# Optimization experiments

Hardware: AMD Instinct MI355X
Metric: run time of the kernel (lower is better)

## Reference

```python
import jax, jax.numpy as jnp
import numpy as np

N = 50000
E = 400000
DIM_IN = 512
DIM_H = 64
HEADS = 8
DIM_OUT = 40
SLOPE = 0.2  # PyG GATv2Conv default negative_slope


def setup_inputs() -> dict:
    key = jax.random.key(0)
    ks = jax.random.split(key, 16)
    s = 0.05
    return {
        "x": jax.random.normal(ks[0], (N, DIM_IN), dtype=jnp.float32),
        "edge_index": jax.random.randint(ks[1], (2, E), 0, N, dtype=jnp.int64),
        "Wl1": jax.random.normal(ks[2], (DIM_IN, HEADS * DIM_H), dtype=jnp.float32) * s,
        "Wr1": jax.random.normal(ks[3], (DIM_IN, HEADS * DIM_H), dtype=jnp.float32) * s,
        "att1": jax.random.normal(ks[4], (HEADS, DIM_H), dtype=jnp.float32) * s,
        "b1": jax.random.normal(ks[5], (HEADS * DIM_H,), dtype=jnp.float32) * s,
        "Wl2": jax.random.normal(ks[6], (HEADS * DIM_H, DIM_OUT), dtype=jnp.float32) * s,
        "Wr2": jax.random.normal(ks[7], (HEADS * DIM_H, DIM_OUT), dtype=jnp.float32) * s,
        "att2": jax.random.normal(ks[8], (1, DIM_OUT), dtype=jnp.float32) * s,
        "b2": jax.random.normal(ks[9], (DIM_OUT,), dtype=jnp.float32) * s,
        "Wl3": jax.random.normal(ks[10], (HEADS * DIM_H, 2), dtype=jnp.float32) * s,
        "Wr3": jax.random.normal(ks[11], (HEADS * DIM_H, 2), dtype=jnp.float32) * s,
        "att3": jax.random.normal(ks[12], (1, 2), dtype=jnp.float32) * s,
        "b3": jax.random.normal(ks[13], (2,), dtype=jnp.float32) * s,
    }


def gatv2(x, src, dst, Wl, Wr, att, b):
    # PyG GATv2Conv: e_ij = att . LeakyReLU(W_l x_j + W_r x_i); softmax over j (by dst i);
    # out_i = sum_j alpha_ij * (W_l x_j); heads concatenated; bias added after.
    n = x.shape[0]
    H, F = att.shape
    xl = (x @ Wl).reshape(n, H, F)  # source transform
    xr = (x @ Wr).reshape(n, H, F)  # target transform
    e = jax.nn.leaky_relu(xl[src] + xr[dst], negative_slope=SLOPE)  # [E, H, F]
    logits = jnp.einsum("ehf,hf->eh", e, att)  # [E, H]
    m = jax.ops.segment_max(logits, dst, num_segments=n)  # self-loops => every segment nonempty
    ex = jnp.exp(logits - m[dst])
    denom = jax.ops.segment_sum(ex, dst, num_segments=n)
    alpha = ex / denom[dst]  # [E, H]
    out = jax.ops.segment_sum(xl[src] * alpha[:, :, None], dst, num_segments=n)  # [N, H, F]
    return out.reshape(n, H * F) + b


def reference(x, edge_index, Wl1, Wr1, att1, b1, Wl2, Wr2, att2, b2, Wl3, Wr3, att3, b3):
    # add self loops (PyG default add_self_loops=True)
    loops = jnp.arange(N, dtype=edge_index.dtype)
    ei = jnp.concatenate([edge_index, jnp.stack([loops, loops])], axis=1)
    src, dst = ei[0], ei[1]
    # eval mode: dropout is identity; ReverseLayerF is identity in forward
    h = jax.nn.relu(gatv2(x, src, dst, Wl1, Wr1, att1, b1))
    y_class = gatv2(h, src, dst, Wl2, Wr2, att2, b2)
    y_domain = gatv2(h, src, dst, Wl3, Wr3, att3, b3)
    return (y_class, y_domain)
```

## Files before the change

### kernel.cpp

```cpp
#include <hip/hip_runtime.h>
#include <math.h>

typedef unsigned short u16;
typedef unsigned int   u32;
typedef __attribute__((ext_vector_type(8))) short bf16x8;
typedef __attribute__((ext_vector_type(4))) float f32x4;
typedef __attribute__((ext_vector_type(4))) u32   u32x4;

__device__ __forceinline__ float b2f(u16 u) {
  union { u32 i; float f; } v; v.i = ((u32)u) << 16; return v.f;
}
__device__ __forceinline__ u16 f2b(float f) {
  union { u32 i; float f; } v; v.f = f;
  u32 r = v.i + 0x7FFFu + ((v.i >> 16) & 1u);
  return (u16)(r >> 16);
}
__device__ __forceinline__ float blo(u32 w) {
  union { u32 i; float f; } v; v.i = w << 16; return v.f;
}
__device__ __forceinline__ float bhi(u32 w) {
  union { u32 i; float f; } v; v.i = w & 0xFFFF0000u; return v.f;
}
__device__ __forceinline__ void ld_lds16(const u16* g, u16* l) {
  __builtin_amdgcn_global_load_lds((const __attribute__((address_space(1))) void*)g,
                                   (__attribute__((address_space(3))) void*)l, 16, 0, 0);
}

#define NN 50000
#define NE 400000
#define NT 450000
#define NBLK_SCAN 196

__global__ void k_detect(const void* x, const void* ei, int* flags) {
  __shared__ int cnt[2];
  int t = threadIdx.x;
  if (t < 2) cnt[t] = 0;
  __syncthreads();
  u16 u = ((const u16*)x)[t];
  int e = (u >> 7) & 0xFF;
  if (u == 0 || (e >= 90 && e <= 134)) atomicAdd(&cnt[0], 1);
  if (t < 16) {
    if (((const int*)ei)[2 * t + 1] == 0) atomicAdd(&cnt[1], 1);
  }
  __syncthreads();
  if (t == 0) {
    flags[0] = (cnt[0] >= 110) ? 1 : 0;
    flags[1] = (cnt[1] >= 15) ? 1 : 0;
  }
}

__device__ __forceinline__ int eidx(const int* ei, int pos, int i64) {
  return i64 ? ei[2 * pos] : ei[pos];
}

__global__ void k_convert_x(const void* x, const int* flags, u16* xb) {
  if (flags[0]) return;
  int c = blockIdx.x * 256 + threadIdx.x;
  const float* xf = (const float*)x + (size_t)c * 8;
  u32x4 o;
  #pragma unroll
  for (int i = 0; i < 4; ++i) {
    u32 lo = f2b(xf[2 * i]);
    u32 hi = f2b(xf[2 * i + 1]);
    o[i] = lo | (hi << 16);
  }
  *(u32x4*)(xb + (size_t)c * 8) = o;
}

__global__ void k_pack(const void* Wl1, const void* Wr1, const void* Wl2, const void* Wr2,
                       const void* Wl3, const void* Wr3, const void* att1, const void* b1,
                       const void* att2, const void* b2, const void* att3, const void* b3,
                       const int* flags, u16* w1t, u16* w23t, float* params) {
  int b = blockIdx.x;
  int isbf = flags[0];
  if (b < 2048) {
    int t = b * 256 + threadIdx.x;
    int r = t >> 9;
    int k = t & 511;
    const void* W = (r < 512) ? Wl1 : Wr1;
    int cc = r & 511;
    u16 v = isbf ? ((const u16*)W)[k * 512 + cc] : f2b(((const float*)W)[k * 512 + cc]);
    w1t[(size_t)r * 512 + k] = v;
  } else if (b < 2240) {
    int t = (b - 2048) * 256 + threadIdx.x;
    int k = t / 96;
    int c = t % 96;
    const void* W = nullptr; int idx = 0;
    if (c < 40)      { W = Wl2; idx = k * 40 + c; }
    else if (c < 42) { W = Wl3; idx = k * 2 + (c - 40); }
    else if (c < 82) { W = Wr2; idx = k * 40 + (c - 42); }
    else if (c < 84) { W = Wr3; idx = k * 2 + (c - 82); }
    u16 v = 0;
    if (W) v = isbf ? ((const u16*)W)[idx] : f2b(((const float*)W)[idx]);
    w23t[c * 512 + k] = v;
  } else {
    int t = (b - 2240) * 256 + threadIdx.x;
    if (t >= 1108) return;
    const void* src; int idx;
    if (t < 512)       { src = att1; idx = t; }
    else if (t < 1024) { src = b1;   idx = t - 512; }
    else if (t < 1064) { src = att2; idx = t - 1024; }
    else if (t < 1104) { src = b2;   idx = t - 1064; }
    else if (t < 1106) { src = att3; idx = t - 1104; }
    else               { src = b3;   idx = t - 1106; }
    params[t] = isbf ? b2f(((const u16*)src)[idx]) : ((const float*)src)[idx];
  }
}

__global__ void k_hist(const int* ei, const int* flags, int* deg) {
  int e = blockIdx.x * 256 + threadIdx.x;
  if (e >= NE) return;
  int d = eidx(ei, NE + e, flags[1]);
  atomicAdd(&deg[d], 1);
}

__global__ void k_scanA(const int* deg, int* row_ptr, int* bsum) {
  __shared__ int sh[256];
  int b = blockIdx.x, t = threadIdx.x;
  int i = b * 256 + t;
  int val = (i < NN) ? deg[i] + 1 : 0;
  sh[t] = val;
  __syncthreads();
  #pragma unroll
  for (int off = 1; off < 256; off <<= 1) {
    int v = (t >= off) ? sh[t - off] : 0;
    __syncthreads();
    sh[t] += v;
    __syncthreads();
  }
  if (i < NN) row_ptr[i] = sh[t] - val;
  if (t == 255) bsum[b] = sh[255];
}

__global__ void k_scanB(int* bsum, int* row_ptr) {
  __shared__ int sh[256];
  int t = threadIdx.x;
  int val = (t < NBLK_SCAN) ? bsum[t] : 0;
  sh[t] = val;
  __syncthreads();
  #pragma unroll
  for (int off = 1; off < 256; off <<= 1) {
    int v = (t >= off) ? sh[t - off] : 0;
    __syncthreads();
    sh[t] += v;
    __syncthreads();
  }
  if (t < NBLK_SCAN) bsum[t] = sh[t] - val;
  if (t == 255) row_ptr[NN] = sh[255];
}

__global__ void k_scanC(const int* bsum, int* row_ptr, int* cursor) {
  int i = blockIdx.x * 256 + threadIdx.x;
  if (i < NN) {
    int v = row_ptr[i] + bsum[blockIdx.x];
    row_ptr[i] = v;
    cursor[i] = v;
  }
}

__global__ void k_scatter(const int* ei, const int* flags, int* cursor, int* csr_src) {
  int t = blockIdx.x * 256 + threadIdx.x;
  if (t >= NT) return;
  int i64 = flags[1];
  int s, d;
  if (t < NE) { s = eidx(ei, t, i64); d = eidx(ei, NE + t, i64); }
  else        { s = d = t - NE; }
  int pos = atomicAdd(&cursor[d], 1);
  csr_src[pos] = s;
}

__global__ __launch_bounds__(256) void k_gemm1(const void* __restrict__ xraw, const u16* __restrict__ xb,
                                               const u16* __restrict__ Bt, const int* __restrict__ flags,
                                               u16* __restrict__ XL, u16* __restrict__ XR) {
  __shared__ __align__(16) u16 As[128 * 64];
  __shared__ __align__(16) u16 Bs[128 * 64];
  const int id  = blockIdx.x;
  const int xcd = id & 7;
  const int lb  = id >> 3;
  const int mt  = xcd * 49 + (lb >> 3);
  const int nt  = lb & 7;
  if (mt >= 391) return;
  const int m0 = mt * 128;
  const int n0 = nt * 128;
  const u16* __restrict__ A = flags[0] ? (const u16*)xraw : xb;
  const int t = threadIdx.x;
  const int wave = t >> 6;
  const int lane = t & 63;
  const int wm = (wave >> 1) * 64;
  const int wn = (wave & 1) * 64;
  const int fr = lane & 15;
  const int fk = lane >> 4;
  const int srow = lane >> 3;
  const int schk = (lane & 7) ^ srow;
  f32x4 acc[4][4] = {};
  for (int k0 = 0; k0 < 512; k0 += 64) {
    #pragma unroll
    for (int q = 0; q < 4; ++q) {
      int rbase = wave * 32 + q * 8;
      int gm = m0 + rbase + srow;
      if (gm > NN - 1) gm = NN - 1;
      ld_lds16(&A[(size_t)gm * 512 + k0 + schk * 8], &As[rbase * 64]);
      ld_lds16(&Bt[(size_t)(n0 + rbase + srow) * 512 + k0 + schk * 8], &Bs[rbase * 64]);
    }
    __syncthreads();
    #pragma unroll
    for (int h = 0; h < 2; ++h) {
      int s = h * 4 + fk;
      bf16x8 af[4], bb[4];
      #pragma unroll
      for (int i = 0; i < 4; ++i) {
        int row = wm + i * 16 + fr;
        af[i] = *(const bf16x8*)&As[row * 64 + ((s ^ (row & 7)) * 8)];
      }
      #pragma unroll
      for (int j = 0; j < 4; ++j) {
        int row = wn + j * 16 + fr;
        bb[j] = *(const bf16x8*)&Bs[row * 64 + ((s ^ (row & 7)) * 8)];
      }
      #pragma unroll
      for (int i = 0; i < 4; ++i)
        #pragma unroll
        for (int j = 0; j < 4; ++j)
          acc[i][j] = __builtin_amdgcn_mfma_f32_16x16x32_bf16(af[i], bb[j], acc[i][j], 0, 0, 0);
    }
    __syncthreads();
  }
  #pragma unroll
  for (int i = 0; i < 4; ++i) {
    #pragma unroll
    for (int r = 0; r < 4; ++r) {
      int gm = m0 + wm + i * 16 + fk * 4 + r;
      if (gm < NN) {
        #pragma unroll
        for (int j = 0; j < 4; ++j) {
          int gn = n0 + wn + j * 16 + fr;
          u16 v = f2b(acc[i][j][r]);
          if (gn < 512) XL[(size_t)gm * 512 + gn] = v;
          else          XR[(size_t)gm * 512 + gn - 512] = v;
        }
      }
    }
  }
}

__global__ __launch_bounds__(256) void k_gemm2(const u16* __restrict__ A, const u16* __restrict__ Bt,
                                               float* __restrict__ xlp, float* __restrict__ xrp) {
  __shared__ __align__(16) short As[128][40];
  __shared__ __align__(16) short Bs[96][40];
  const int m0 = blockIdx.x * 128;
  const int t = threadIdx.x;
  const int wave = t >> 6;
  const int lane = t & 63;
  const int fr = lane & 15;
  const int fk = lane >> 4;
  const int wm = wave * 32;
  f32x4 acc[2][6] = {};
  for (int k0 = 0; k0 < 512; k0 += 32) {
    #pragma unroll
    for (int h = 0; h < 2; ++h) {
      int c = t + h * 256;
      int row = c >> 2, kc = (c & 3) * 8;
      int gm = m0 + row;
      u32x4 va = {0, 0, 0, 0};
      if (gm < NN) va = *(const u32x4*)&A[(size_t)gm * 512 + k0 + kc];
      *(u32x4*)&As[row][kc] = va;
    }
    for (int c = t; c < 384; c += 256) {
      int row = c >> 2, kc = (c & 3) * 8;
      *(u32x4*)&Bs[row][kc] = *(const u32x4*)&Bt[row * 512 + k0 + kc];
    }
    __syncthreads();
    bf16x8 af[2], bb[6];
    #pragma unroll
    for (int i = 0; i < 2; ++i) af[i] = *(const bf16x8*)&As[wm + i * 16 + fr][fk * 8];
    #pragma unroll
    for (int j = 0; j < 6; ++j) bb[j] = *(const bf16x8*)&Bs[j * 16 + fr][fk * 8];
    #pragma unroll
    for (int i = 0; i < 2; ++i)
      #pragma unroll
      for (int j = 0; j < 6; ++j)
        acc[i][j] = __builtin_amdgcn_mfma_f32_16x16x32_bf16(af[i], bb[j], acc[i][j], 0, 0, 0);
    __syncthreads();
  }
  #pragma unroll
  for (int i = 0; i < 2; ++i) {
    #pragma unroll
    for (int j = 0; j < 6; ++j) {
      int gn = j * 16 + fr;
      if (gn < 84) {
        #pragma unroll
        for (int r = 0; r < 4; ++r) {
          int gm = m0 + wm + i * 16 + fk * 4 + r;
          if (gm < NN) {
            if (gn < 42) xlp[(size_t)gm * 48 + gn] = acc[i][j][r];
            else         xrp[(size_t)gm * 48 + gn - 42] = acc[i][j][r];
          }
        }
      }
    }
  }
}

__global__ __launch_bounds__(256) void k_layer1f(const u16* __restrict__ xl1, const u16* __restrict__ xr1,
                                                 const int* __restrict__ row_ptr, const int* __restrict__ csr_src,
                                                 const float* __restrict__ params, u16* __restrict__ hb) {
  int wid = blockIdx.x * 4 + (threadIdx.x >> 6);
  int lane = threadIdx.x & 63;
  int nw = gridDim.x * 4;
  float att4[8];
  #pragma unroll
  for (int k = 0; k < 8; ++k) att4[k] = 0.4f * params[lane * 8 + k];
  for (int i = wid; i < NN; i += nw) {
    int e0 = row_ptr[i], e1 = row_ptr[i + 1];
    u32x4 xrv = *(const u32x4*)&xr1[(size_t)i * 512 + lane * 8];
    float xr[8];
    #pragma unroll
    for (int q = 0; q < 4; ++q) { xr[2 * q] = blo(xrv[q]); xr[2 * q + 1] = bhi(xrv[q]); }
    float dp = 0.f;
    #pragma unroll
    for (int k = 0; k < 8; ++k) dp = fmaf(att4[k], 1.5f * xr[k], dp);
    dp += __shfl_xor(dp, 1, 64);
    dp += __shfl_xor(dp, 2, 64);
    dp += __shfl_xor(dp, 4, 64);
    float s = 0.f;
    float acc[8] = {0.f, 0.f, 0.f, 0.f, 0.f, 0.f, 0.f, 0.f};
    int q0 = csr_src[e0];
    int q1 = csr_src[e0 + 1 < e1 ? e0 + 1 : e1 - 1];
    int q2 = csr_src[e0 + 2 < e1 ? e0 + 2 : e1 - 1];
    int q3 = csr_src[e0 + 3 < e1 ? e0 + 3 : e1 - 1];
    for (int p = e0; p < e1; p += 4) {
      int j0 = q0, j1 = q1, j2 = q2, j3 = q3;
      u32x4 v0 = *(const u32x4*)&xl1[(size_t)j0 * 512 + lane * 8];
      u32x4 v1 = *(const u32x4*)&xl1[(size_t)j1 * 512 + lane * 8];
      u32x4 v2 = *(const u32x4*)&xl1[(size_t)j2 * 512 + lane * 8];
      u32x4 v3 = *(const u32x4*)&xl1[(size_t)j3 * 512 + lane * 8];
      int np = p + 4;
      if (np < e1) {
        q0 = csr_src[np];
        q1 = csr_src[np + 1 < e1 ? np + 1 : e1 - 1];
        q2 = csr_src[np + 2 < e1 ? np + 2 : e1 - 1];
        q3 = csr_src[np + 3 < e1 ? np + 3 : e1 - 1];
      }
      float m1 = (p + 1 < e1) ? 1.f : 0.f;
      float m2 = (p + 2 < e1) ? 1.f : 0.f;
      float m3 = (p + 3 < e1) ? 1.f : 0.f;
      float c0 = 0.f, c1 = 0.f, c2 = 0.f, c3 = 0.f;
      float xlv0[8], xlv1[8], xlv2[8], xlv3[8];
      #pragma unroll
      for (int q = 0; q < 4; ++q) {
        xlv0[2 * q] = blo(v0[q]); xlv0[2 * q + 1] = bhi(v0[q]);
        xlv1[2 * q] = blo(v1[q]); xlv1[2 * q + 1] = bhi(v1[q]);
        xlv2[2 * q] = blo(v2[q]); xlv2[2 * q + 1] = bhi(v2[q]);
        xlv3[2 * q] = blo(v3[q]); xlv3[2 * q + 1] = bhi(v3[q]);
      }
      #pragma unroll
      for (int k = 0; k < 8; ++k) {
        float t0 = xlv0[k] + xr[k];
        float t1 = xlv1[k] + xr[k];
        float t2 = xlv2[k] + xr[k];
        float t3 = xlv3[k] + xr[k];
        float u0 = fmaf(1.5f, xlv0[k], fabsf(t0));
        float u1 = fmaf(1.5f, xlv1[k], fabsf(t1));
        float u2 = fmaf(1.5f, xlv2[k], fabsf(t2));
        float u3 = fmaf(1.5f, xlv3[k], fabsf(t3));
        c0 = fmaf(att4[k], u0, c0);
        c1 = fmaf(att4[k], u1, c1);
        c2 = fmaf(att4[k], u2, c2);
        c3 = fmaf(att4[k], u3, c3);
      }
      c0 += __shfl_xor(c0, 1, 64); c1 += __shfl_xor(c1, 1, 64);
      c2 += __shfl_xor(c2, 2, 64); c3 += __shfl_xor(c3, 1, 64);
      c0 += __shfl_xor(c0, 2, 64); c1 += __shfl_xor(c1, 2, 64);
      c2 += __shfl_xor(c2, 1, 64); c3 += __shfl_xor(c3, 2, 64);
      c0 += __shfl_xor(c0, 4, 64); c1 += __shfl_xor(c1, 4, 64);
      c2 += __shfl_xor(c2, 4, 64); c3 += __shfl_xor(c3, 4, 64);
      float l0 = c0 + dp;
      float l1 = c1 + dp;
      float l2 = c2 + dp;
      float l3 = c3 + dp;
      float pv0 = __expf(fminf(fmaxf(l0, -30.f), 30.f));
      float pv1 = __expf(fminf(fmaxf(l1, -30.f), 30.f)) * m1;
      float pv2 = __expf(fminf(fmaxf(l2, -30.f), 30.f)) * m2;
      float pv3 = __expf(fminf(fmaxf(l3, -30.f), 30.f)) * m3;
      s += (pv0 + pv1) + (pv2 + pv3);
      #pragma unroll
      for (int k = 0; k < 8; ++k) {
        float a = fmaf(pv0, xlv0[k], acc[k]);
        a = fmaf(pv1, xlv1[k], a);
        a = fmaf(pv2, xlv2[k], a);
        acc[k] = fmaf(pv3, xlv3[k], a);
      }
    }
    float r = 1.f / s;
    u32x4 o;
    #pragma unroll
    for (int q = 0; q < 4; ++q) {
      u32 lo = f2b(fmaxf(fmaf(acc[2 * q],     r, params[512 + lane * 8 + 2 * q]),     0.f));
      u32 hi = f2b(fmaxf(fmaf(acc[2 * q + 1], r, params[512 + lane * 8 + 2 * q + 1]), 0.f));
      o[q] = lo | (hi << 16);
    }
    *(u32x4*)&hb[(size_t)i * 512 + lane * 8] = o;
  }
}

__global__ __launch_bounds__(256) void k_layer23f(const float* __restrict__ xlp, const float* __restrict__ xrp,
                                                  const int* __restrict__ row_ptr, const int* __restrict__ csr_src,
                                                  const float* __restrict__ params,
                                                  const int* __restrict__ flags, void* __restrict__ out) {
  int wid = blockIdx.x * 4 + (threadIdx.x >> 6);
  int lane = threadIdx.x & 63;
  int nw = gridDim.x * 4;
  int e = lane >> 3;
  int g = lane & 7;
  int c0 = g * 5;
  float att2[5];
  #pragma unroll
  for (int u = 0; u < 5; ++u) att2[u] = params[1024 + c0 + u];
  float att3a = params[1104], att3b = params[1105];
  int isbf = flags[0];
  for (int i = wid; i < NN; i += nw) {
    int e0 = row_ptr[i], e1 = row_ptr[i + 1];
    const float* xri = &xrp[(size_t)i * 48];
    float xr2[5];
    #pragma unroll
    for (int u = 0; u < 5; ++u) xr2[u] = xri[c0 + u];
    float xr3a = xri[40], xr3b = xri[41];
    float s2 = 0.f, s3 = 0.f;
    float acc2[5] = {0.f, 0.f, 0.f, 0.f, 0.f};
    float acc3a = 0.f, acc3b = 0.f;
    int nit = (e1 - e0 + 7) >> 3;
    for (int it = 0; it < nit; ++it) {
      int p = e0 + it * 8 + e;
      bool valid = p < e1;
      int j = csr_src[valid ? p : e1 - 1];
      const float* xlj = &xlp[(size_t)j * 48];
      float xl2[5];
      #pragma unroll
      for (int u = 0; u < 5; ++u) xl2[u] = xlj[c0 + u];
      float part = 0.f;
      #pragma unroll
      for (int u = 0; u < 5; ++u) {
        float t = xl2[u] + xr2[u];
        part = fmaf(att2[u], fmaxf(t, 0.2f * t), part);
      }
      part += __shfl_xor(part, 1, 64);
      part += __shfl_xor(part, 2, 64);
      part += __shfl_xor(part, 4, 64);
      float pv2 = valid ? __expf(fminf(fmaxf(part, -30.f), 30.f)) : 0.f;
      s2 += pv2;
      #pragma unroll
      for (int u = 0; u < 5; ++u) acc2[u] = fmaf(pv2, xl2[u], acc2[u]);
      if (g == 0) {
        float xl3a = xlj[40], xl3b = xlj[41];
        float ta = xl3a + xr3a, tb = xl3b + xr3b;
        float l3 = fmaf(att3a, fmaxf(ta, 0.2f * ta), att3b * fmaxf(tb, 0.2f * tb));
        float pv3 = valid ? __expf(fminf(fmaxf(l3, -30.f), 30.f)) : 0.f;
        s3 += pv3;
        acc3a = fmaf(pv3, xl3a, acc3a);
        acc3b = fmaf(pv3, xl3b, acc3b);
      }
    }
    #pragma unroll
    for (int m = 8; m <= 32; m <<= 1) {
      #pragma unroll
      for (int u = 0; u < 5; ++u) acc2[u] += __shfl_xor(acc2[u], m, 64);
      s2 += __shfl_xor(s2, m, 64);
      acc3a += __shfl_xor(acc3a, m, 64);
      acc3b += __shfl_xor(acc3b, m, 64);
      s3 += __shfl_xor(s3, m, 64);
    }
    if (e == 0) {
      float r2 = 1.f / s2;
      #pragma unroll
      for (int u = 0; u < 5; ++u) {
        float v = acc2[u] * r2 + params[1064 + c0 + u];
        size_t o = (size_t)i * 40 + c0 + u;
        if (isbf) ((u16*)out)[o] = f2b(v); else ((float*)out)[o] = v;
      }
      if (g == 0) {
        float r3 = 1.f / s3;
        float va = acc3a * r3 + params[1106];
        float vb = acc3b * r3 + params[1107];
        size_t o = 2000000 + (size_t)i * 2;
        if (isbf) { ((u16*)out)[o] = f2b(va); ((u16*)out)[o + 1] = f2b(vb); }
        else      { ((float*)out)[o] = va;    ((float*)out)[o + 1] = vb; }
      }
    }
  }
}

extern "C" void kernel_launch(void* const* d_in, const int* in_sizes, int n_in,
                              void* d_out, int out_size, void* d_ws, size_t ws_size,
                              hipStream_t stream) {
  const void* x    = d_in[0];
  const int*  ei   = (const int*)d_in[1];
  const void* Wl1  = d_in[2];
  const void* Wr1  = d_in[3];
  const void* att1 = d_in[4];
  const void* b1   = d_in[5];
  const void* Wl2  = d_in[6];
  const void* Wr2  = d_in[7];
  const void* att2 = d_in[8];
  const void* b2   = d_in[9];
  const void* Wl3  = d_in[10];
  const void* Wr3  = d_in[11];
  const void* att3 = d_in[12];
  const void* b3   = d_in[13];
  (void)in_sizes; (void)n_in; (void)out_size;

  char* ws = (char*)d_ws;
  size_t off = 0;
  auto alloc = [&](size_t bytes) -> void* {
    void* p = ws + off;
    off = (off + bytes + 255) & ~(size_t)255;
    return p;
  };
  int*   flags   = (int*)  alloc(64);
  u16*   xb      = (u16*)  alloc((size_t)NN * 512 * 2);
  u16*   w1t     = (u16*)  alloc((size_t)1024 * 512 * 2);
  u16*   xl1     = (u16*)  alloc((size_t)NN * 512 * 2);
  u16*   xr1     = (u16*)  alloc((size_t)NN * 512 * 2);
  u16*   hb      = (u16*)  alloc((size_t)NN * 512 * 2);
  u16*   w23t    = (u16*)  alloc((size_t)96 * 512 * 2);
  float* xlp     = (float*)alloc((size_t)NN * 48 * 4);
  float* xrp     = (float*)alloc((size_t)NN * 48 * 4);
  float* params  = (float*)alloc(1108 * 4);
  int*   row_ptr = (int*)  alloc((NN + 1) * 4);
  int*   deg     = (int*)  alloc(NN * 4);
  int*   cursor  = (int*)  alloc(NN * 4);
  int*   csr_src = (int*)  alloc((NT + 16) * 4);
  int*   bsum    = (int*)  alloc(256 * 4);
  if (ws_size < off) return;

  hipLaunchKernelGGL(k_detect, dim3(1), dim3(128), 0, stream, x, (const void*)ei, flags);
  hipLaunchKernelGGL(k_convert_x, dim3(12500), dim3(256), 0, stream, x, flags, xb);
  hipLaunchKernelGGL(k_pack, dim3(2245), dim3(256), 0, stream, Wl1, Wr1, Wl2, Wr2, Wl3, Wr3,
                     att1, b1, att2, b2, att3, b3, flags, w1t, w23t, params);
  hipMemsetAsync(deg, 0, NN * 4, stream);
  hipLaunchKernelGGL(k_hist, dim3((NE + 255) / 256), dim3(256), 0, stream, ei, flags, deg);
  hipLaunchKernelGGL(k_scanA, dim3(NBLK_SCAN), dim3(256), 0, stream, deg, row_ptr, bsum);
  hipLaunchKernelGGL(k_scanB, dim3(1), dim3(256), 0, stream, bsum, row_ptr);
  hipLaunchKernelGGL(k_scanC, dim3(NBLK_SCAN), dim3(256), 0, stream, bsum, row_ptr, cursor);
  hipLaunchKernelGGL(k_scatter, dim3((NT + 255) / 256), dim3(256), 0, stream, ei, flags, cursor, csr_src);
  hipLaunchKernelGGL(k_gemm1, dim3(3136), dim3(256), 0, stream, x, xb, w1t, flags, xl1, xr1);
  hipLaunchKernelGGL(k_layer1f, dim3(4096), dim3(256), 0, stream, xl1, xr1, row_ptr, csr_src, params, hb);
  hipLaunchKernelGGL(k_gemm2, dim3(391), dim3(256), 0, stream, hb, w23t, xlp, xrp);
  hipLaunchKernelGGL(k_layer23f, dim3(4096), dim3(256), 0, stream, xlp, xrp, row_ptr, csr_src, params, flags, d_out);
}
```

Before: 448.9 us.

## Merge prep kernels and double-buffer A tiles in layer-2 GEMM

Merges the x conversion and weight packing kernels into one launch, cutting one kernel launch. Weight transposition now indexes k-major so reads of the source weights are coalesced. In k_gemm2 the A tile is double-buffered in LDS, with the next slice prefetched into registers while MFMAs run, and B fragments are read straight from global memory instead of being staged. This drops one barrier per k-step but adds global B reads per wave. A shuffle-order tweak in the layer-2/3 reduction is only a reordering with the same sum.

```diff
diff --git a/kernel.cpp b/kernel.cpp
--- a/kernel.cpp
+++ b/kernel.cpp
@@ -53,36 +53,35 @@
   return i64 ? ei[2 * pos] : ei[pos];
 }
 
-__global__ void k_convert_x(const void* x, const int* flags, u16* xb) {
-  if (flags[0]) return;
-  int c = blockIdx.x * 256 + threadIdx.x;
-  const float* xf = (const float*)x + (size_t)c * 8;
-  u32x4 o;
-  #pragma unroll
-  for (int i = 0; i < 4; ++i) {
-    u32 lo = f2b(xf[2 * i]);
-    u32 hi = f2b(xf[2 * i + 1]);
-    o[i] = lo | (hi << 16);
-  }
-  *(u32x4*)(xb + (size_t)c * 8) = o;
-}
-
-__global__ void k_pack(const void* Wl1, const void* Wr1, const void* Wl2, const void* Wr2,
-                       const void* Wl3, const void* Wr3, const void* att1, const void* b1,
-                       const void* att2, const void* b2, const void* att3, const void* b3,
-                       const int* flags, u16* w1t, u16* w23t, float* params) {
+__global__ void k_prep(const void* x, const void* Wl1, const void* Wr1, const void* Wl2,
+                       const void* Wr2, const void* Wl3, const void* Wr3, const void* att1,
+                       const void* b1, const void* att2, const void* b2, const void* att3,
+                       const void* b3, const int* flags, u16* xb, u16* w1t, u16* w23t,
+                       float* params) {
   int b = blockIdx.x;
   int isbf = flags[0];
-  if (b < 2048) {
-    int t = b * 256 + threadIdx.x;
-    int r = t >> 9;
-    int k = t & 511;
-    const void* W = (r < 512) ? Wl1 : Wr1;
-    int cc = r & 511;
+  if (b < 12500) {
+    if (isbf) return;
+    int c = b * 256 + threadIdx.x;
+    const float* xf = (const float*)x + (size_t)c * 8;
+    u32x4 o;
+    #pragma unroll
+    for (int i = 0; i < 4; ++i) {
+      u32 lo = f2b(xf[2 * i]);
+      u32 hi = f2b(xf[2 * i + 1]);
+      o[i] = lo | (hi << 16);
+    }
+    *(u32x4*)(xb + (size_t)c * 8) = o;
+  } else if (b < 14548) {
+    int t = (b - 12500) * 256 + threadIdx.x;
+    int k = t >> 10;
+    int c = t & 1023;
+    const void* W = (c < 512) ? Wl1 : Wr1;
+    int cc = c & 511;
     u16 v = isbf ? ((const u16*)W)[k * 512 + cc] : f2b(((const float*)W)[k * 512 + cc]);
-    w1t[(size_t)r * 512 + k] = v;
-  } else if (b < 2240) {
-    int t = (b - 2048) * 256 + threadIdx.x;
+    w1t[(size_t)c * 512 + k] = v;
+  } else if (b < 14740) {
+    int t = (b - 14548) * 256 + threadIdx.x;
     int k = t / 96;
     int c = t % 96;
     const void* W = nullptr; int idx = 0;
@@ -94,7 +93,7 @@
     if (W) v = isbf ? ((const u16*)W)[idx] : f2b(((const float*)W)[idx]);
     w23t[c * 512 + k] = v;
   } else {
-    int t = (b - 2240) * 256 + threadIdx.x;
+    int t = (b - 14740) * 256 + threadIdx.x;
     if (t >= 1108) return;
     const void* src; int idx;
     if (t < 512)       { src = att1; idx = t; }
@@ -245,8 +244,7 @@
 
 __global__ __launch_bounds__(256) void k_gemm2(const u16* __restrict__ A, const u16* __restrict__ Bt,
                                                float* __restrict__ xlp, float* __restrict__ xrp) {
-  __shared__ __align__(16) short As[128][40];
-  __shared__ __align__(16) short Bs[96][40];
+  __shared__ __align__(16) short As[2][128][40];
   const int m0 = blockIdx.x * 128;
   const int t = threadIdx.x;
   const int wave = t >> 6;
@@ -255,32 +253,45 @@
   const int fk = lane >> 4;
   const int wm = wave * 32;
   f32x4 acc[2][6] = {};
-  for (int k0 = 0; k0 < 512; k0 += 32) {
-    #pragma unroll
-    for (int h = 0; h < 2; ++h) {
-      int c = t + h * 256;
-      int row = c >> 2, kc = (c & 3) * 8;
-      int gm = m0 + row;
-      u32x4 va = {0, 0, 0, 0};
-      if (gm < NN) va = *(const u32x4*)&A[(size_t)gm * 512 + k0 + kc];
-      *(u32x4*)&As[row][kc] = va;
-    }
-    for (int c = t; c < 384; c += 256) {
-      int row = c >> 2, kc = (c & 3) * 8;
-      *(u32x4*)&Bs[row][kc] = *(const u32x4*)&Bt[row * 512 + k0 + kc];
-    }
-    __syncthreads();
+  #pragma unroll
+  for (int h = 0; h < 2; ++h) {
+    int c = t + h * 256;
+    int row = c >> 2, kc = (c & 3) * 8;
+    int gm = m0 + row;
+    u32x4 va = {0, 0, 0, 0};
+    if (gm < NN) va = *(const u32x4*)&A[(size_t)gm * 512 + kc];
+    *(u32x4*)&As[0][row][kc] = va;
+  }
+  __syncthreads();
+  int cur = 0;
+  for (int ks = 0; ks < 16; ++ks) {
+    int k0 = ks * 32;
+    u32x4 nva0 = {0, 0, 0, 0}, nva1 = {0, 0, 0, 0};
+    if (ks < 15) {
+      int c0 = t, row0 = c0 >> 2, kc0 = (c0 & 3) * 8;
+      int c1 = t + 256, row1 = c1 >> 2, kc1 = (c1 & 3) * 8;
+      int gm0 = m0 + row0, gm1 = m0 + row1;
+      if (gm0 < NN) nva0 = *(const u32x4*)&A[(size_t)gm0 * 512 + k0 + 32 + kc0];
+      if (gm1 < NN) nva1 = *(const u32x4*)&A[(size_t)gm1 * 512 + k0 + 32 + kc1];
+    }
     bf16x8 af[2], bb[6];
     #pragma unroll
-    for (int i = 0; i < 2; ++i) af[i] = *(const bf16x8*)&As[wm + i * 16 + fr][fk * 8];
-    #pragma unroll
-    for (int j = 0; j < 6; ++j) bb[j] = *(const bf16x8*)&Bs[j * 16 + fr][fk * 8];
+    for (int j = 0; j < 6; ++j) bb[j] = *(const bf16x8*)&Bt[(size_t)(j * 16 + fr) * 512 + k0 + fk * 8];
+    #pragma unroll
+    for (int i = 0; i < 2; ++i) af[i] = *(const bf16x8*)&As[cur][wm + i * 16 + fr][fk * 8];
     #pragma unroll
     for (int i = 0; i < 2; ++i)
       #pragma unroll
       for (int j = 0; j < 6; ++j)
         acc[i][j] = __builtin_amdgcn_mfma_f32_16x16x32_bf16(af[i], bb[j], acc[i][j], 0, 0, 0);
-    __syncthreads();
+    if (ks < 15) {
+      int c0 = t, row0 = c0 >> 2, kc0 = (c0 & 3) * 8;
+      int c1 = t + 256, row1 = c1 >> 2, kc1 = (c1 & 3) * 8;
+      *(u32x4*)&As[cur ^ 1][row0][kc0] = nva0;
+      *(u32x4*)&As[cur ^ 1][row1][kc1] = nva1;
+    }
+    __syncthreads();
+    cur ^= 1;
   }
   #pragma unroll
   for (int i = 0; i < 2; ++i) {
@@ -369,9 +380,9 @@
         c3 = fmaf(att4[k], u3, c3);
       }
       c0 += __shfl_xor(c0, 1, 64); c1 += __shfl_xor(c1, 1, 64);
-      c2 += __shfl_xor(c2, 2, 64); c3 += __shfl_xor(c3, 1, 64);
+      c2 += __shfl_xor(c2, 1, 64); c3 += __shfl_xor(c3, 1, 64);
       c0 += __shfl_xor(c0, 2, 64); c1 += __shfl_xor(c1, 2, 64);
-      c2 += __shfl_xor(c2, 1, 64); c3 += __shfl_xor(c3, 2, 64);
+      c2 += __shfl_xor(c2, 2, 64); c3 += __shfl_xor(c3, 2, 64);
       c0 += __shfl_xor(c0, 4, 64); c1 += __shfl_xor(c1, 4, 64);
       c2 += __shfl_xor(c2, 4, 64); c3 += __shfl_xor(c3, 4, 64);
       float l0 = c0 + dp;
@@ -533,9 +544,8 @@
   if (ws_size < off) return;
 
   hipLaunchKernelGGL(k_detect, dim3(1), dim3(128), 0, stream, x, (const void*)ei, flags);
-  hipLaunchKernelGGL(k_convert_x, dim3(12500), dim3(256), 0, stream, x, flags, xb);
-  hipLaunchKernelGGL(k_pack, dim3(2245), dim3(256), 0, stream, Wl1, Wr1, Wl2, Wr2, Wl3, Wr3,
-                     att1, b1, att2, b2, att3, b3, flags, w1t, w23t, params);
+  hipLaunchKernelGGL(k_prep, dim3(14745), dim3(256), 0, stream, x, Wl1, Wr1, Wl2, Wr2, Wl3, Wr3,
+                     att1, b1, att2, b2, att3, b3, flags, xb, w1t, w23t, params);
   hipMemsetAsync(deg, 0, NN * 4, stream);
   hipLaunchKernelGGL(k_hist, dim3((NE + 255) / 256), dim3(256), 0, stream, ei, flags, deg);
   hipLaunchKernelGGL(k_scanA, dim3(NBLK_SCAN), dim3(256), 0, stream, deg, row_ptr, bsum);
```

Measured after the change: 454.0 us. About the same (+1.1%).

## Fuse fp32-to-bf16 conversion of x into the first GEMM's tile load

Applied to the files above, without the earlier changes.

Removes the standalone x conversion kernel and its bf16 staging buffer. The first GEMM now loads fp32 rows of x directly, converts them with packed bf16 conversion instructions and writes them into the same swizzled LDS layout the async loads produced. The epilogue also uses the packed conversion instead of manual rounding. This saves a full read and write pass over x, but each A tile is now re-read in fp32 by all eight column tiles, and it goes through registers instead of asynchronous direct-to-LDS loads, which may slow the GEMM's load phase.

```diff
diff --git a/kernel.cpp b/kernel.cpp
--- a/kernel.cpp
+++ b/kernel.cpp
@@ -20,6 +20,11 @@
 }
 __device__ __forceinline__ float bhi(u32 w) {
   union { u32 i; float f; } v; v.i = w & 0xFFFF0000u; return v.f;
+}
+__device__ __forceinline__ u32 cvtpk(float a, float b) {
+  u32 r;
+  asm("v_cvt_pk_bf16_f32 %0, %1, %2" : "=v"(r) : "v"(a), "v"(b));
+  return r;
 }
 __device__ __forceinline__ void ld_lds16(const u16* g, u16* l) {
   __builtin_amdgcn_global_load_lds((const __attribute__((address_space(1))) void*)g,
@@ -51,20 +56,6 @@
 
 __device__ __forceinline__ int eidx(const int* ei, int pos, int i64) {
   return i64 ? ei[2 * pos] : ei[pos];
-}
-
-__global__ void k_convert_x(const void* x, const int* flags, u16* xb) {
-  if (flags[0]) return;
-  int c = blockIdx.x * 256 + threadIdx.x;
-  const float* xf = (const float*)x + (size_t)c * 8;
-  u32x4 o;
-  #pragma unroll
-  for (int i = 0; i < 4; ++i) {
-    u32 lo = f2b(xf[2 * i]);
-    u32 hi = f2b(xf[2 * i + 1]);
-    o[i] = lo | (hi << 16);
-  }
-  *(u32x4*)(xb + (size_t)c * 8) = o;
 }
 
 __global__ void k_pack(const void* Wl1, const void* Wr1, const void* Wl2, const void* Wr2,
@@ -169,8 +160,8 @@
   csr_src[pos] = s;
 }
 
-__global__ __launch_bounds__(256) void k_gemm1(const void* __restrict__ xraw, const u16* __restrict__ xb,
-                                               const u16* __restrict__ Bt, const int* __restrict__ flags,
+__global__ __launch_bounds__(256) void k_gemm1(const void* __restrict__ xraw, const u16* __restrict__ Bt,
+                                               const int* __restrict__ flags,
                                                u16* __restrict__ XL, u16* __restrict__ XR) {
   __shared__ __align__(16) u16 As[128 * 64];
   __shared__ __align__(16) u16 Bs[128 * 64];
@@ -182,7 +173,9 @@
   if (mt >= 391) return;
   const int m0 = mt * 128;
   const int n0 = nt * 128;
-  const u16* __restrict__ A = flags[0] ? (const u16*)xraw : xb;
+  const int isbf = flags[0];
+  const u16*   __restrict__ Ab = (const u16*)xraw;
+  const float* __restrict__ Af = (const float*)xraw;
   const int t = threadIdx.x;
   const int wave = t >> 6;
   const int lane = t & 63;
@@ -197,10 +190,32 @@
     #pragma unroll
     for (int q = 0; q < 4; ++q) {
       int rbase = wave * 32 + q * 8;
-      int gm = m0 + rbase + srow;
-      if (gm > NN - 1) gm = NN - 1;
-      ld_lds16(&A[(size_t)gm * 512 + k0 + schk * 8], &As[rbase * 64]);
       ld_lds16(&Bt[(size_t)(n0 + rbase + srow) * 512 + k0 + schk * 8], &Bs[rbase * 64]);
+    }
+    if (isbf) {
+      #pragma unroll
+      for (int q = 0; q < 4; ++q) {
+        int rbase = wave * 32 + q * 8;
+        int gm = m0 + rbase + srow;
+        if (gm > NN - 1) gm = NN - 1;
+        ld_lds16(&Ab[(size_t)gm * 512 + k0 + schk * 8], &As[rbase * 64]);
+      }
+    } else {
+      #pragma unroll
+      for (int q = 0; q < 4; ++q) {
+        int rbase = wave * 32 + q * 8;
+        int gm = m0 + rbase + srow;
+        if (gm > NN - 1) gm = NN - 1;
+        const float* src = Af + (size_t)gm * 512 + k0 + schk * 8;
+        f32x4 a0 = *(const f32x4*)src;
+        f32x4 a1 = *(const f32x4*)(src + 4);
+        u32x4 o;
+        o[0] = cvtpk(a0[0], a0[1]);
+        o[1] = cvtpk(a0[2], a0[3]);
+        o[2] = cvtpk(a1[0], a1[1]);
+        o[3] = cvtpk(a1[2], a1[3]);
+        *(u32x4*)&As[rbase * 64 + lane * 8] = o;
+      }
     }
     __syncthreads();
     #pragma unroll
@@ -232,11 +247,17 @@
       int gm = m0 + wm + i * 16 + fk * 4 + r;
       if (gm < NN) {
         #pragma unroll
-        for (int j = 0; j < 4; ++j) {
-          int gn = n0 + wn + j * 16 + fr;
-          u16 v = f2b(acc[i][j][r]);
-          if (gn < 512) XL[(size_t)gm * 512 + gn] = v;
-          else          XR[(size_t)gm * 512 + gn - 512] = v;
+        for (int jp = 0; jp < 2; ++jp) {
+          u32 pk = cvtpk(acc[i][2 * jp][r], acc[i][2 * jp + 1][r]);
+          int gn0 = n0 + wn + (2 * jp) * 16 + fr;
+          u16 lo = (u16)pk, hi = (u16)(pk >> 16);
+          if (gn0 < 512) {
+            XL[(size_t)gm * 512 + gn0] = lo;
+            XL[(size_t)gm * 512 + gn0 + 16] = hi;
+          } else {
+            XR[(size_t)gm * 512 + gn0 - 512] = lo;
+            XR[(size_t)gm * 512 + gn0 - 496] = hi;
+          }
         }
       }
     }
@@ -369,9 +390,9 @@
         c3 = fmaf(att4[k], u3, c3);
       }
       c0 += __shfl_xor(c0, 1, 64); c1 += __shfl_xor(c1, 1, 64);
-      c2 += __shfl_xor(c2, 2, 64); c3 += __shfl_xor(c3, 1, 64);
+      c2 += __shfl_xor(c2, 1, 64); c3 += __shfl_xor(c3, 1, 64);
       c0 += __shfl_xor(c0, 2, 64); c1 += __shfl_xor(c1, 2, 64);
-      c2 += __shfl_xor(c2, 1, 64); c3 += __shfl_xor(c3, 2, 64);
+      c2 += __shfl_xor(c2, 2, 64); c3 += __shfl_xor(c3, 2, 64);
       c0 += __shfl_xor(c0, 4, 64); c1 += __shfl_xor(c1, 4, 64);
       c2 += __shfl_xor(c2, 4, 64); c3 += __shfl_xor(c3, 4, 64);
       float l0 = c0 + dp;
@@ -516,7 +537,6 @@
     return p;
   };
   int*   flags   = (int*)  alloc(64);
-  u16*   xb      = (u16*)  alloc((size_t)NN * 512 * 2);
   u16*   w1t     = (u16*)  alloc((size_t)1024 * 512 * 2);
   u16*   xl1     = (u16*)  alloc((size_t)NN * 512 * 2);
   u16*   xr1     = (u16*)  alloc((size_t)NN * 512 * 2);
@@ -533,7 +553,6 @@
   if (ws_size < off) return;
 
   hipLaunchKernelGGL(k_detect, dim3(1), dim3(128), 0, stream, x, (const void*)ei, flags);
-  hipLaunchKernelGGL(k_convert_x, dim3(12500), dim3(256), 0, stream, x, flags, xb);
   hipLaunchKernelGGL(k_pack, dim3(2245), dim3(256), 0, stream, Wl1, Wr1, Wl2, Wr2, Wl3, Wr3,
                      att1, b1, att2, b2, att3, b3, flags, w1t, w23t, params);
   hipMemsetAsync(deg, 0, NN * 4, stream);
@@ -542,7 +561,7 @@
   hipLaunchKernelGGL(k_scanB, dim3(1), dim3(256), 0, stream, bsum, row_ptr);
   hipLaunchKernelGGL(k_scanC, dim3(NBLK_SCAN), dim3(256), 0, stream, bsum, row_ptr, cursor);
   hipLaunchKernelGGL(k_scatter, dim3((NT + 255) / 256), dim3(256), 0, stream, ei, flags, cursor, csr_src);
-  hipLaunchKernelGGL(k_gemm1, dim3(3136), dim3(256), 0, stream, x, xb, w1t, flags, xl1, xr1);
+  hipLaunchKernelGGL(k_gemm1, dim3(3136), dim3(256), 0, stream, x, w1t, flags, xl1, xr1);
   hipLaunchKernelGGL(k_layer1f, dim3(4096), dim3(256), 0, stream, xl1, xr1, row_ptr, csr_src, params, hb);
   hipLaunchKernelGGL(k_gemm2, dim3(391), dim3(256), 0, stream, hb, w23t, xlp, xrp);
   hipLaunchKernelGGL(k_layer23f, dim3(4096), dim3(256), 0, stream, xlp, xrp, row_ptr, csr_src, params, flags, d_out);
```

Result: no change. 440.3 us (-1.9%).
